# Kernel tuning notes

Measured on AMD Instinct MI355X. Metric: run time of the kernel, lower is better.

The kernel has to match this reference:

```python
import jax, jax.numpy as jnp
import numpy as np

BS, D, NC, N, C, K = 8192, 1024, 64, 100000, 1000, 50


def setup_inputs() -> dict:
    key = jax.random.key(0)
    k1, k2, k3, k4, k5 = jax.random.split(key, 5)
    return {
        "train_embedding": jax.random.normal(k1, (BS, D), dtype=jnp.float32),
        # concept initialized uniform in [-0.5, 0.5] as in init_concept
        "concept": jax.random.uniform(k2, (D, NC), dtype=jnp.float32, minval=-0.5, maxval=0.5),
        "bank": jax.random.normal(k3, (N, D), dtype=jnp.float32),
        "W_h": jax.random.normal(k4, (D, C), dtype=jnp.float32) * 0.02,
        "b_h": jax.random.normal(k5, (C,), dtype=jnp.float32) * 0.02,
        "topk": K,
    }


def reference(train_embedding, concept, bank, W_h, b_h, topk):
    # h_x: linear classifier head
    def h_x(z):
        return z @ W_h + b_h

    # projection onto concept subspace: C (C^T C)^{-1} C^T
    G = concept.T @ concept                      # [nc, nc]
    proj_matrix = concept @ jnp.linalg.inv(G) @ concept.T  # [D, D]
    proj = train_embedding @ proj_matrix.T       # (proj_matrix @ X^T)^T -> [bs, D]
    y_pred = h_x(proj)                           # [bs, C]
    orig_pred = h_x(train_embedding)             # [bs, C]

    # batched per-concept Euclidean distance to the whole bank: [nc, N]
    bank_sq = jnp.sum(bank * bank, axis=1)       # [N]
    con_sq = jnp.sum(concept * concept, axis=0)  # [nc]
    d2 = con_sq[:, None] - 2.0 * (concept.T @ bank.T) + bank_sq[None, :]
    dist = jnp.sqrt(jnp.maximum(d2, 0.0))
    # topk SMALLEST distances per concept
    _, idx = jax.lax.top_k(-dist, topk)          # idx: [nc, k]
    knn = bank[idx]                              # [nc, k, D] gather

    # L_sparse_1: mean over concepts of (c . mean_k knn)
    dots = jnp.einsum('dn,nkd->n', concept, knn) / topk  # [nc]
    L_sparse_1 = jnp.mean(dots)

    nc = concept.shape[1]
    eye = jnp.eye(nc, dtype=concept.dtype)
    L_sparse_2 = jnp.mean(G * (1.0 - eye))       # off-diagonal mean
    norm_metrics = jnp.mean(G * eye)             # diagonal mean

    return (orig_pred, y_pred, L_sparse_1, L_sparse_2, norm_metrics)
```

## Files before the change

### kernel.cpp

```cpp
#include <hip/hip_runtime.h>
#include <cstddef>

#define BSZ   8192
#define DIM   1024
#define NCON  64
#define NBANK 100000
#define NCLS  1000
#define TOPK  50
#define NCHUNK 32
#define CHUNK  3125
#define CHUNKP 3328

#define Y_OFF 8192000
#define S_OFF 16384000

typedef __attribute__((ext_vector_type(8))) short bf16x8;
typedef __attribute__((ext_vector_type(4))) float f32x4;

__device__ __forceinline__ short f2bf(float x) {
    unsigned u = __builtin_bit_cast(unsigned, x);
    unsigned r = (u + 0x7fffu + ((u >> 16) & 1u)) >> 16;
    return (short)r;
}

__device__ __forceinline__ bf16x8 pack8(f32x4 a, f32x4 b) {
    bf16x8 p;
    p[0] = f2bf(a[0]); p[1] = f2bf(a[1]); p[2] = f2bf(a[2]); p[3] = f2bf(a[3]);
    p[4] = f2bf(b[0]); p[5] = f2bf(b[1]); p[6] = f2bf(b[2]); p[7] = f2bf(b[3]);
    return p;
}

__device__ __forceinline__ void gload16(const short* g, short* l) {
    __builtin_amdgcn_global_load_lds(
        (__attribute__((address_space(1))) void*)g,
        (__attribute__((address_space(3))) void*)l,
        16, 0, 0);
}

__global__ void __launch_bounds__(256) prep_kernel(const float* __restrict__ X,
                                                   const float* __restrict__ cpt,
                                                   const float* __restrict__ Wh,
                                                   short* __restrict__ Xbf,
                                                   short* __restrict__ WcatT,
                                                   short* __restrict__ cptT,
                                                   short* __restrict__ cptR) {
    __shared__ short Ts[64][65];
    int b = blockIdx.x;
    int t = threadIdx.x;
    if (b < 4096) {
        size_t u = ((size_t)b * 256 + t) * 8;
        f32x4 a = *(const f32x4*)(X + u);
        f32x4 c = *(const f32x4*)(X + u + 4);
        *(bf16x8*)(Xbf + u) = pack8(a, c);
    } else if (b < 4352) {
        int q = b - 4096;
        int k0 = (q & 15) * 64, n0 = (q >> 4) * 64;
        #pragma unroll
        for (int i = 0; i < 16; ++i) {
            int u = i * 256 + t;
            int kL = u >> 6, nL = u & 63;
            int n = n0 + nL;
            Ts[kL][nL] = (n < NCLS) ? f2bf(Wh[(size_t)(k0 + kL) * NCLS + n]) : (short)0;
        }
        __syncthreads();
        #pragma unroll
        for (int i = 0; i < 16; ++i) {
            int u = i * 256 + t;
            int nL = u >> 6, kL = u & 63;
            WcatT[(size_t)(n0 + nL) * DIM + k0 + kL] = Ts[kL][nL];
        }
    } else {
        int q = b - 4352;
        #pragma unroll
        for (int i = 0; i < 16; ++i) {
            int u = q * 4096 + i * 256 + t;
            int d = u >> 6, n = u & 63;
            short v = f2bf(cpt[u]);
            cptR[u] = v;
            cptT[n * DIM + d] = v;
        }
    }
}

__global__ void __launch_bounds__(256) mid_kernel(const float* __restrict__ bank,
                                                  const short* __restrict__ cptT,
                                                  const short* __restrict__ WcatT,
                                                  float* __restrict__ key,
                                                  float* __restrict__ bank_sq,
                                                  float* __restrict__ M,
                                                  float* __restrict__ G,
                                                  float* __restrict__ invG) {
    __shared__ float rowk[64];
    __shared__ float fk[64];
    int b = blockIdx.x;
    int t = threadIdx.x;
    int wid = t >> 6, l = t & 63, lr = l & 15, lg = l >> 4;
    if (b < 782) {
        int j0 = b * 128;
        int j_[2]; bool v_[2];
        const float* brow[2];
        #pragma unroll
        for (int ni = 0; ni < 2; ++ni) {
            j_[ni] = j0 + wid * 32 + ni * 16 + lr;
            v_[ni] = j_[ni] < NBANK;
            brow[ni] = bank + (size_t)j_[ni] * DIM + lg * 8;
        }
        f32x4 acc[4][2] = {};
        float sq[2] = {0.f, 0.f};
        for (int kk = 0; kk < DIM; kk += 32) {
            bf16x8 af[4];
            #pragma unroll
            for (int mi = 0; mi < 4; ++mi)
                af[mi] = *(const bf16x8*)(cptT + (mi * 16 + lr) * DIM + kk + lg * 8);
            #pragma unroll
            for (int ni = 0; ni < 2; ++ni) {
                f32x4 a = v_[ni] ? *(const f32x4*)(brow[ni] + kk)     : f32x4{0.f, 0.f, 0.f, 0.f};
                f32x4 c = v_[ni] ? *(const f32x4*)(brow[ni] + kk + 4) : f32x4{0.f, 0.f, 0.f, 0.f};
                sq[ni] += a[0]*a[0] + a[1]*a[1] + a[2]*a[2] + a[3]*a[3]
                        + c[0]*c[0] + c[1]*c[1] + c[2]*c[2] + c[3]*c[3];
                bf16x8 bfr = pack8(a, c);
                #pragma unroll
                for (int mi = 0; mi < 4; ++mi)
                    acc[mi][ni] = __builtin_amdgcn_mfma_f32_16x16x32_bf16(af[mi], bfr, acc[mi][ni], 0, 0, 0);
            }
        }
        #pragma unroll
        for (int ni = 0; ni < 2; ++ni) {
            float s = sq[ni];
            s += __shfl_xor(s, 16);
            s += __shfl_xor(s, 32);
            sq[ni] = s;
            if (v_[ni] && lg == 0) bank_sq[j_[ni]] = s;
        }
        #pragma unroll
        for (int mi = 0; mi < 4; ++mi)
            #pragma unroll
            for (int ni = 0; ni < 2; ++ni)
                if (v_[ni]) {
                    #pragma unroll
                    for (int r = 0; r < 4; ++r) {
                        int m = mi * 16 + lg * 4 + r;
                        key[(size_t)m * NBANK + j_[ni]] = sq[ni] - 2.f * acc[mi][ni][r];
                    }
                }
    } else if (b < 790) {
        int c0 = (b - 782) * 128;
        f32x4 acc[4][2] = {};
        for (int kk = 0; kk < DIM; kk += 32) {
            bf16x8 af[4], bfr[2];
            #pragma unroll
            for (int mi = 0; mi < 4; ++mi)
                af[mi] = *(const bf16x8*)(cptT + (mi * 16 + lr) * DIM + kk + lg * 8);
            #pragma unroll
            for (int ni = 0; ni < 2; ++ni)
                bfr[ni] = *(const bf16x8*)(WcatT + (size_t)(c0 + wid * 32 + ni * 16 + lr) * DIM + kk + lg * 8);
            #pragma unroll
            for (int mi = 0; mi < 4; ++mi)
                #pragma unroll
                for (int ni = 0; ni < 2; ++ni)
                    acc[mi][ni] = __builtin_amdgcn_mfma_f32_16x16x32_bf16(af[mi], bfr[ni], acc[mi][ni], 0, 0, 0);
        }
        #pragma unroll
        for (int mi = 0; mi < 4; ++mi)
            #pragma unroll
            for (int ni = 0; ni < 2; ++ni)
                #pragma unroll
                for (int r = 0; r < 4; ++r)
                    M[(mi * 16 + lg * 4 + r) * 1024 + c0 + wid * 32 + ni * 16 + lr] = acc[mi][ni][r];
    } else {
        f32x4 acc[4] = {};
        for (int kk = 0; kk < DIM; kk += 32) {
            bf16x8 af[4], bfr;
            #pragma unroll
            for (int mi = 0; mi < 4; ++mi)
                af[mi] = *(const bf16x8*)(cptT + (mi * 16 + lr) * DIM + kk + lg * 8);
            bfr = *(const bf16x8*)(cptT + (wid * 16 + lr) * DIM + kk + lg * 8);
            #pragma unroll
            for (int mi = 0; mi < 4; ++mi)
                acc[mi] = __builtin_amdgcn_mfma_f32_16x16x32_bf16(af[mi], bfr, acc[mi], 0, 0, 0);
        }
        #pragma unroll
        for (int mi = 0; mi < 4; ++mi)
            #pragma unroll
            for (int r = 0; r < 4; ++r)
                G[(mi * 16 + lg * 4 + r) * 64 + wid * 16 + lr] = acc[mi][r];
        __syncthreads();
        float myA[16];
        #pragma unroll
        for (int s = 0; s < 16; ++s) myA[s] = G[(4 * s + wid) * 64 + l];
        #pragma unroll
        for (int k = 0; k < 64; ++k) {
            if (wid == (k & 3)) rowk[l] = myA[k >> 2];
            if (l == k) {
                #pragma unroll
                for (int s = 0; s < 16; ++s) fk[4 * s + wid] = myA[s];
            }
            __syncthreads();
            float ip = 1.f / rowk[k];
            float rv = rowk[l];
            #pragma unroll
            for (int s = 0; s < 16; ++s) {
                int i = 4 * s + wid;
                float fv = fk[i];
                float nv;
                if (i == k && l == k)      nv = ip;
                else if (i == k)           nv = rv * ip;
                else if (l == k)           nv = -fv * ip;
                else                       nv = myA[s] - fv * (rv * ip);
                myA[s] = nv;
            }
            __syncthreads();
        }
        #pragma unroll
        for (int s = 0; s < 16; ++s) invG[(4 * s + wid) * 64 + l] = myA[s];
    }
}

__global__ void __launch_bounds__(256) topA_kernel(const float* __restrict__ key,
                                                   float* __restrict__ cand_v,
                                                   int* __restrict__ cand_j) {
    int n = blockIdx.x >> 5;
    int c = blockIdx.x & 31;
    int base = c * CHUNK;
    const float* row = key + (size_t)n * NBANK + base;
    __shared__ float vals[CHUNKP];
    __shared__ float wv[4];
    __shared__ int wj[4];
    int t = threadIdx.x;
    float lv = __builtin_inff();
    int lj = 0x7fffffff;
    #pragma unroll 13
    for (int i = 0; i < 13; ++i) {
        int j = t + i * 256;
        float v = (j < CHUNK) ? row[j] : __builtin_inff();
        vals[j] = v;
        if (v < lv) { lv = v; lj = j; }
    }
    __syncthreads();
    float* cv = cand_v + (size_t)blockIdx.x * TOPK;
    int* cj = cand_j + (size_t)blockIdx.x * TOPK;
    for (int it = 0; it < TOPK; ++it) {
        float bv = lv; int bj = lj;
        #pragma unroll
        for (int o = 32; o > 0; o >>= 1) {
            float ov = __shfl_down(bv, o);
            int oj = __shfl_down(bj, o);
            if (ov < bv || (ov == bv && oj < bj)) { bv = ov; bj = oj; }
        }
        if ((t & 63) == 0) { wv[t >> 6] = bv; wj[t >> 6] = bj; }
        __syncthreads();
        float gv = wv[0]; int gj = wj[0];
        #pragma unroll
        for (int w = 1; w < 4; ++w)
            if (wv[w] < gv || (wv[w] == gv && wj[w] < gj)) { gv = wv[w]; gj = wj[w]; }
        if (t == 0) { cv[it] = gv; cj[it] = base + gj; }
        if (t == (gj & 255)) {
            vals[gj] = __builtin_inff();
            lv = __builtin_inff(); lj = 0x7fffffff;
            #pragma unroll 13
            for (int i = 0; i < 13; ++i) {
                int j = t + i * 256;
                float v = vals[j];
                if (v < lv) { lv = v; lj = j; }
            }
        }
        __syncthreads();
    }
}

__global__ void __launch_bounds__(256) m2w2_topB_kernel(const float* __restrict__ invG,
                                                        const float* __restrict__ M,
                                                        const short* __restrict__ cptR,
                                                        short* __restrict__ WcatT,
                                                        const float* __restrict__ cand_v,
                                                        const int* __restrict__ cand_j,
                                                        const float* __restrict__ bank_sq,
                                                        float* __restrict__ dots) {
    __shared__ __align__(16) char smem[49408];
    int b = blockIdx.x;
    int t = threadIdx.x;
    if (b < 8) {
        float* Mt = (float*)smem;
        short* M2s = (short*)(smem + 33024);
        int c0 = b * 128;
        for (int u = t; u < 8192; u += 256) {
            int j = u >> 7, cc = u & 127;
            Mt[j * 129 + cc] = M[j * 1024 + c0 + cc];
        }
        __syncthreads();
        int cl = t & 127, half = t >> 7;
        for (int nn = 0; nn < 32; ++nn) {
            int n = half * 32 + nn;
            float a = 0.f;
            #pragma unroll 16
            for (int j = 0; j < 64; ++j) a += invG[n * 64 + j] * Mt[j * 129 + cl];
            int s = n >> 3;
            M2s[cl * 64 + (((s ^ (cl & 7)) << 3) | (n & 7))] = f2bf(a);
        }
        __syncthreads();
        int wid = t >> 6, l = t & 63, lr = l & 15, lg = l >> 4;
        int wr = wid >> 1, wc = wid & 1;
        for (int d0 = 0; d0 < DIM; d0 += 128) {
            f32x4 acc[4][4] = {};
            #pragma unroll
            for (int ks = 0; ks < 2; ++ks) {
                bf16x8 af[4], bfr[4];
                #pragma unroll
                for (int mi = 0; mi < 4; ++mi) {
                    int rr = wr * 64 + mi * 16 + lr;
                    int slot = (ks * 4 + lg) ^ (rr & 7);
                    af[mi] = *(const bf16x8*)(M2s + rr * 64 + slot * 8);
                }
                #pragma unroll
                for (int ni = 0; ni < 4; ++ni)
                    bfr[ni] = *(const bf16x8*)(cptR + (size_t)(d0 + wc * 64 + ni * 16 + lr) * 64 + ks * 32 + lg * 8);
                #pragma unroll
                for (int mi = 0; mi < 4; ++mi)
                    #pragma unroll
                    for (int ni = 0; ni < 4; ++ni)
                        acc[mi][ni] = __builtin_amdgcn_mfma_f32_16x16x32_bf16(af[mi], bfr[ni], acc[mi][ni], 0, 0, 0);
            }
            #pragma unroll
            for (int mi = 0; mi < 4; ++mi)
                #pragma unroll
                for (int ni = 0; ni < 4; ++ni)
                    #pragma unroll
                    for (int r = 0; r < 4; ++r) {
                        int cc = c0 + wr * 64 + mi * 16 + lg * 4 + r;
                        int d = d0 + wc * 64 + ni * 16 + lr;
                        WcatT[(size_t)(1024 + cc) * DIM + d] = f2bf(acc[mi][ni][r]);
                    }
        }
    } else {
        int n = b - 8;
        const int NC2 = NCHUNK * TOPK;
        float* vals = (float*)smem;
        int* gidx = (int*)(smem + 6400);
        float* wv = (float*)(smem + 12800);
        int* wj = (int*)(smem + 12816);
        int* wl = (int*)(smem + 12832);
        for (int j = t; j < NC2; j += 256) {
            vals[j] = cand_v[(size_t)n * NC2 + j];
            gidx[j] = cand_j[(size_t)n * NC2 + j];
        }
        __syncthreads();
        float sum = 0.f;
        for (int it = 0; it < TOPK; ++it) {
            float bv = __builtin_inff();
            int bj = 0x7fffffff;
            int bl = -1;
            #pragma unroll 7
            for (int j = t; j < NC2; j += 256) {
                float v = vals[j];
                int gj = gidx[j];
                if (v < bv || (v == bv && gj < bj)) { bv = v; bj = gj; bl = j; }
            }
            #pragma unroll
            for (int o = 32; o > 0; o >>= 1) {
                float ov = __shfl_down(bv, o);
                int oj = __shfl_down(bj, o);
                int ol = __shfl_down(bl, o);
                if (ov < bv || (ov == bv && oj < bj)) { bv = ov; bj = oj; bl = ol; }
            }
            if ((t & 63) == 0) { wv[t >> 6] = bv; wj[t >> 6] = bj; wl[t >> 6] = bl; }
            __syncthreads();
            if (t == 0) {
                #pragma unroll
                for (int w = 1; w < 4; ++w)
                    if (wv[w] < bv || (wv[w] == bv && wj[w] < bj)) { bv = wv[w]; bj = wj[w]; bl = wl[w]; }
                sum += 0.5f * (bank_sq[bj] - bv);
                vals[bl] = __builtin_inff();
            }
            __syncthreads();
        }
        if (t == 0) dots[n] = sum / (float)TOPK;
    }
}

__global__ void __launch_bounds__(256) pred_fin_kernel(const short* __restrict__ Xbf,
                                                       const short* __restrict__ WcatT,
                                                       const float* __restrict__ bh,
                                                       const float* __restrict__ G,
                                                       const float* __restrict__ dots,
                                                       float* __restrict__ orig,
                                                       float* __restrict__ ypred,
                                                       float* __restrict__ out3) {
    __shared__ __align__(16) char smem[32768];
    int b = blockIdx.x;
    int t = threadIdx.x;
    if (b < 1024) {
        short* As = (short*)smem;
        short* Bs = (short*)(smem + 16384);
        int c0 = (b & 15) * 128;
        int r0 = (b >> 4) * 128;
        int wid = t >> 6, l = t & 63, lr = l & 15, lg = l >> 4;
        int wr = wid >> 1, wc = wid & 1;
        int srow_off = l >> 3;
        int scol = ((l & 7) ^ (l >> 3)) * 8;
        f32x4 acc[4][4] = {};
        for (int kk = 0; kk < DIM; kk += 64) {
            if (kk) __syncthreads();
            #pragma unroll
            for (int i = 0; i < 4; ++i) {
                int si = wid * 4 + i;
                int row = si * 8 + srow_off;
                gload16(Xbf + (size_t)(r0 + row) * DIM + kk + scol, As + si * 512);
                gload16(WcatT + (size_t)(c0 + row) * DIM + kk + scol, Bs + si * 512);
            }
            __syncthreads();
            #pragma unroll
            for (int ks = 0; ks < 2; ++ks) {
                bf16x8 af[4], bfr[4];
                #pragma unroll
                for (int mi = 0; mi < 4; ++mi) {
                    int rr = wr * 64 + mi * 16 + lr;
                    int slot = (ks * 4 + lg) ^ (rr & 7);
                    af[mi] = *(const bf16x8*)(As + rr * 64 + slot * 8);
                }
                #pragma unroll
                for (int ni = 0; ni < 4; ++ni) {
                    int cc = wc * 64 + ni * 16 + lr;
                    int slot = (ks * 4 + lg) ^ (cc & 7);
                    bfr[ni] = *(const bf16x8*)(Bs + cc * 64 + slot * 8);
                }
                #pragma unroll
                for (int mi = 0; mi < 4; ++mi)
                    #pragma unroll
                    for (int ni = 0; ni < 4; ++ni)
                        acc[mi][ni] = __builtin_amdgcn_mfma_f32_16x16x32_bf16(af[mi], bfr[ni], acc[mi][ni], 0, 0, 0);
            }
        }
        #pragma unroll
        for (int mi = 0; mi < 4; ++mi)
            #pragma unroll
            for (int ni = 0; ni < 4; ++ni) {
                int cg = c0 + wc * 64 + ni * 16 + lr;
                bool isorig = cg < NCLS;
                bool isy = (cg >= 1024) && (cg < 1024 + NCLS);
                if (isorig || isy) {
                    int cl = isorig ? cg : cg - 1024;
                    float bias = bh[cl];
                    float* dst = isorig ? orig : ypred;
                    #pragma unroll
                    for (int r = 0; r < 4; ++r) {
                        int row = r0 + wr * 64 + mi * 16 + lg * 4 + r;
                        dst[(size_t)row * NCLS + cl] = acc[mi][ni][r] + bias;
                    }
                }
            }
    } else {
        float* r1 = (float*)smem;
        float* r2 = (float*)(smem + 1024);
        float* r3 = (float*)(smem + 2048);
        float sd = 0.f, so = 0.f;
        for (int u = t; u < 4096; u += 256) {
            float g = G[u];
            if ((u >> 6) == (u & 63)) sd += g; else so += g;
        }
        float s1 = (t < NCON) ? dots[t] : 0.f;
        r1[t] = sd; r2[t] = so; r3[t] = s1;
        __syncthreads();
        for (int o = 128; o > 0; o >>= 1) {
            if (t < o) { r1[t] += r1[t + o]; r2[t] += r2[t + o]; r3[t] += r3[t + o]; }
            __syncthreads();
        }
        if (t == 0) {
            out3[0] = r3[0] / 64.f;
            out3[1] = r2[0] / 4096.f;
            out3[2] = r1[0] / 4096.f;
        }
    }
}

extern "C" void kernel_launch(void* const* d_in, const int* in_sizes, int n_in,
                              void* d_out, int out_size, void* d_ws, size_t ws_size,
                              hipStream_t stream) {
    const float* X    = (const float*)d_in[0];
    const float* cpt  = (const float*)d_in[1];
    const float* bank = (const float*)d_in[2];
    const float* Wh   = (const float*)d_in[3];
    const float* bh   = (const float*)d_in[4];
    float* out = (float*)d_out;

    float* orig  = out;
    float* ypred = out + Y_OFF;
    float* out3  = out + S_OFF;

    char* w = (char*)d_ws;
    short* Xbf    = (short*)(w);
    short* WcatT  = (short*)(w + 16777216);
    short* cptT   = (short*)(w + 20971520);
    short* cptR   = (short*)(w + 21102592);
    float* key    = (float*)(w + 21233664);
    float* bank_sq= (float*)(w + 46833664);
    float* G      = (float*)(w + 47234048);
    float* invG   = (float*)(w + 47250432);
    float* M      = (float*)(w + 47266816);
    float* cand_v = (float*)(w + 47528960);
    int*   cand_j = (int*)  (w + 47938560);
    float* dots   = (float*)(w + 48348160);

    prep_kernel<<<4368, 256, 0, stream>>>(X, cpt, Wh, Xbf, WcatT, cptT, cptR);
    mid_kernel<<<791, 256, 0, stream>>>(bank, cptT, WcatT, key, bank_sq, M, G, invG);
    topA_kernel<<<NCON * NCHUNK, 256, 0, stream>>>(key, cand_v, cand_j);
    m2w2_topB_kernel<<<72, 256, 0, stream>>>(invG, M, cptR, WcatT, cand_v, cand_j, bank_sq, dots);
    pred_fin_kernel<<<1025, 256, 0, stream>>>(Xbf, WcatT, bh, G, dots, orig, ypred, out3);
}
```

Measured before the change: 440.8 us.

## Use single-wave register-resident top-k chunks with more, smaller chunks

The first-stage top-k kernel now gives each 64-thread block (one wavefront) a chunk of about 1563 distances held in registers instead of shared memory. Each of the 50 selection steps uses only wave shuffles, with no __syncthreads or cross-wave reduction. Doubling the chunk count doubles the candidates that the second-stage merge kernel must scan, and the workspace offsets are enlarged to match. The dynamic indexing into the register array is unrolled into compare-and-select chains, which may add instructions or register pressure.

```diff
diff --git a/kernel.cpp b/kernel.cpp
--- a/kernel.cpp
+++ b/kernel.cpp
@@ -7,9 +7,8 @@
 #define NBANK 100000
 #define NCLS  1000
 #define TOPK  50
-#define NCHUNK 32
-#define CHUNK  3125
-#define CHUNKP 3328
+#define NCH2  64
+#define CH2   1563
 
 #define Y_OFF 8192000
 #define S_OFF 16384000
@@ -216,27 +215,25 @@
     }
 }
 
-__global__ void __launch_bounds__(256) topA_kernel(const float* __restrict__ key,
-                                                   float* __restrict__ cand_v,
-                                                   int* __restrict__ cand_j) {
-    int n = blockIdx.x >> 5;
-    int c = blockIdx.x & 31;
-    int base = c * CHUNK;
+__global__ void __launch_bounds__(64) topA_kernel(const float* __restrict__ key,
+                                                  float* __restrict__ cand_v,
+                                                  int* __restrict__ cand_j) {
+    int n = blockIdx.x >> 6;
+    int c = blockIdx.x & 63;
+    int base = c * CH2;
     const float* row = key + (size_t)n * NBANK + base;
-    __shared__ float vals[CHUNKP];
-    __shared__ float wv[4];
-    __shared__ int wj[4];
     int t = threadIdx.x;
+    float r[25];
     float lv = __builtin_inff();
     int lj = 0x7fffffff;
-    #pragma unroll 13
-    for (int i = 0; i < 13; ++i) {
-        int j = t + i * 256;
-        float v = (j < CHUNK) ? row[j] : __builtin_inff();
-        vals[j] = v;
+    #pragma unroll
+    for (int i = 0; i < 25; ++i) {
+        int j = t + i * 64;
+        bool ok = (j < CH2) && (base + j < NBANK);
+        float v = ok ? row[j] : __builtin_inff();
+        r[i] = v;
         if (v < lv) { lv = v; lj = j; }
     }
-    __syncthreads();
     float* cv = cand_v + (size_t)blockIdx.x * TOPK;
     int* cj = cand_j + (size_t)blockIdx.x * TOPK;
     for (int it = 0; it < TOPK; ++it) {
@@ -247,24 +244,18 @@
             int oj = __shfl_down(bj, o);
             if (ov < bv || (ov == bv && oj < bj)) { bv = ov; bj = oj; }
         }
-        if ((t & 63) == 0) { wv[t >> 6] = bv; wj[t >> 6] = bj; }
-        __syncthreads();
-        float gv = wv[0]; int gj = wj[0];
-        #pragma unroll
-        for (int w = 1; w < 4; ++w)
-            if (wv[w] < gv || (wv[w] == gv && wj[w] < gj)) { gv = wv[w]; gj = wj[w]; }
-        if (t == 0) { cv[it] = gv; cj[it] = base + gj; }
-        if (t == (gj & 255)) {
-            vals[gj] = __builtin_inff();
+        bv = __shfl(bv, 0);
+        bj = __shfl(bj, 0);
+        if (t == 0) { cv[it] = bv; cj[it] = base + bj; }
+        if ((bj & 63) == t) {
             lv = __builtin_inff(); lj = 0x7fffffff;
-            #pragma unroll 13
-            for (int i = 0; i < 13; ++i) {
-                int j = t + i * 256;
-                float v = vals[j];
-                if (v < lv) { lv = v; lj = j; }
-            }
-        }
-        __syncthreads();
+            #pragma unroll
+            for (int i = 0; i < 25; ++i) {
+                if (t + i * 64 == bj) r[i] = __builtin_inff();
+                float v = r[i];
+                if (v < lv) { lv = v; lj = t + i * 64; }
+            }
+        }
     }
 }
 
@@ -333,12 +324,12 @@
         }
     } else {
         int n = b - 8;
-        const int NC2 = NCHUNK * TOPK;
+        const int NC2 = NCH2 * TOPK;
         float* vals = (float*)smem;
-        int* gidx = (int*)(smem + 6400);
-        float* wv = (float*)(smem + 12800);
-        int* wj = (int*)(smem + 12816);
-        int* wl = (int*)(smem + 12832);
+        int* gidx = (int*)(smem + 12800);
+        float* wv = (float*)(smem + 25600);
+        int* wj = (int*)(smem + 25616);
+        int* wl = (int*)(smem + 25632);
         for (int j = t; j < NC2; j += 256) {
             vals[j] = cand_v[(size_t)n * NC2 + j];
             gidx[j] = cand_j[(size_t)n * NC2 + j];
@@ -349,7 +340,6 @@
             float bv = __builtin_inff();
             int bj = 0x7fffffff;
             int bl = -1;
-            #pragma unroll 7
             for (int j = t; j < NC2; j += 256) {
                 float v = vals[j];
                 int gj = gidx[j];
@@ -497,12 +487,12 @@
     float* invG   = (float*)(w + 47250432);
     float* M      = (float*)(w + 47266816);
     float* cand_v = (float*)(w + 47528960);
-    int*   cand_j = (int*)  (w + 47938560);
-    float* dots   = (float*)(w + 48348160);
+    int*   cand_j = (int*)  (w + 48348160);
+    float* dots   = (float*)(w + 49167360);
 
     prep_kernel<<<4368, 256, 0, stream>>>(X, cpt, Wh, Xbf, WcatT, cptT, cptR);
     mid_kernel<<<791, 256, 0, stream>>>(bank, cptT, WcatT, key, bank_sq, M, G, invG);
-    topA_kernel<<<NCON * NCHUNK, 256, 0, stream>>>(key, cand_v, cand_j);
+    topA_kernel<<<NCON * NCH2, 64, 0, stream>>>(key, cand_v, cand_j);
     m2w2_topB_kernel<<<72, 256, 0, stream>>>(invG, M, cptR, WcatT, cand_v, cand_j, bank_sq, dots);
     pred_fin_kernel<<<1025, 256, 0, stream>>>(Xbf, WcatT, bh, G, dots, orig, ypred, out3);
 }
```

Result: slower. 463.0 us (+5.0%).
